# Performance work log

Hardware: AMD Instinct MI355X
Metric: run time of the kernel (lower is better)

## Reference

```python
import jax, jax.numpy as jnp
import numpy as np

N_HEADS = 8
HEAD_C = 48
NC = N_HEADS * HEAD_C  # 384
N_GROUPS = 4
GC = NC // N_GROUPS  # 96
STRIDE = 2
EPS = 1e-5


def conv1x1(x, w, b):
    # x: (B,C,H,W), w: (O,C), b: (O,)
    return jnp.einsum('bchw,oc->bohw', x, w) + b[None, :, None, None]


def ref_points(Hk, Wk, dtype):
    ry = jnp.linspace(0.5, Hk - 0.5, Hk, dtype=dtype) / (Hk - 1.0) * 2.0 - 1.0
    rx = jnp.linspace(0.5, Wk - 0.5, Wk, dtype=dtype) / (Wk - 1.0) * 2.0 - 1.0
    return jnp.stack(jnp.meshgrid(ry, rx, indexing='ij'), axis=-1)  # (Hk,Wk,2) in (y,x)


def grid_sample_bilinear(img, grid):
    # img: (N,C,H,W); grid: (N,Hg,Wg,2) xy in [-1,1]; align_corners=True, zeros padding
    N, C, H, W = img.shape
    gx = (grid[..., 0] + 1.0) * 0.5 * (W - 1)
    gy = (grid[..., 1] + 1.0) * 0.5 * (H - 1)
    x0 = jnp.floor(gx); y0 = jnp.floor(gy)
    x1 = x0 + 1.0;      y1 = y0 + 1.0
    wx1 = gx - x0; wx0 = 1.0 - wx1
    wy1 = gy - y0; wy0 = 1.0 - wy1

    def gather(ix, iy):
        valid = (ix >= 0) & (ix <= W - 1) & (iy >= 0) & (iy <= H - 1)
        ixc = jnp.clip(ix, 0, W - 1).astype(jnp.int32)
        iyc = jnp.clip(iy, 0, H - 1).astype(jnp.int32)
        vals = jax.vmap(lambda im, yy, xx: im[:, yy, xx])(img, iyc, ixc)  # (N,C,Hg,Wg)
        return vals * valid[:, None].astype(img.dtype)

    v00 = gather(x0, y0); v01 = gather(x1, y0)
    v10 = gather(x0, y1); v11 = gather(x1, y1)
    return (v00 * (wx0 * wy0)[:, None] + v01 * (wx1 * wy0)[:, None]
            + v10 * (wx0 * wy1)[:, None] + v11 * (wx1 * wy1)[:, None])


def _forward(x, Wq, bq, Wk, bk, Wv, bv, Wo, bo,
             off_dw_w, off_dw_b, ln_g, ln_b, off_pw_w):
    B, C, H, W = x.shape
    q = conv1x1(x, Wq, bq)                               # (B,C,H,W)
    q_off = q.reshape(B * N_GROUPS, GC, H, W)
    # offset net: depthwise 3x3 stride-2 conv -> channel LN -> GELU -> 1x1 to 2 ch
    h = jax.lax.conv_general_dilated(
        q_off, off_dw_w, (STRIDE, STRIDE), ((1, 1), (1, 1)),
        dimension_numbers=('NCHW', 'OIHW', 'NCHW'), feature_group_count=GC)
    h = h + off_dw_b[None, :, None, None]
    mu = h.mean(axis=1, keepdims=True)
    var = ((h - mu) ** 2).mean(axis=1, keepdims=True)
    h = (h - mu) / jnp.sqrt(var + EPS) * ln_g[None, :, None, None] + ln_b[None, :, None, None]
    h = jax.nn.gelu(h, approximate=False)
    offset = jnp.einsum('bchw,oc->bohw', h, off_pw_w)    # (B*g, 2, Hk, Wk), ch0=y, ch1=x
    Hk, Wk_ = offset.shape[2], offset.shape[3]
    rng = jnp.array([1.0 / (Hk - 1.0), 1.0 / (Wk_ - 1.0)], x.dtype).reshape(1, 2, 1, 1)
    offset = jnp.tanh(offset) * rng                      # offset_range_factor = 1
    offset = offset.transpose(0, 2, 3, 1)                # (B*g, Hk, Wk, 2) yx
    ref = ref_points(Hk, Wk_, x.dtype)                   # (Hk, Wk, 2) yx
    pos = offset + ref[None]
    xs = grid_sample_bilinear(x.reshape(B * N_GROUPS, GC, H, W), pos[..., ::-1])
    n = Hk * Wk_
    xs = xs.reshape(B, C, 1, n)
    k = conv1x1(xs, Wk, bk).reshape(B * N_HEADS, HEAD_C, n)
    v = conv1x1(xs, Wv, bv).reshape(B * N_HEADS, HEAD_C, n)
    qh = q.reshape(B * N_HEADS, HEAD_C, H * W)
    attn = jnp.einsum('bcm,bcn->bmn', qh, k) * (HEAD_C ** -0.5)
    attn = jax.nn.softmax(attn, axis=2)
    out = jnp.einsum('bmn,bcn->bcm', attn, v).reshape(B, C, H, W)
    y = conv1x1(out, Wo, bo)
    ref_b = jnp.broadcast_to(ref[None, None], (B, N_GROUPS, Hk, Wk_, 2))
    return y, pos.reshape(B, N_GROUPS, Hk, Wk_, 2), ref_b


def setup_inputs() -> dict:
    key = jax.random.key(0)
    ks = jax.random.split(key, 12)
    s = 0.02
    return {
        'x': jax.random.normal(ks[0], (8, NC, 56, 56), jnp.float32),
        'Wq': jax.random.normal(ks[1], (NC, NC), jnp.float32) * s,
        'bq': jnp.zeros((NC,), jnp.float32),
        'Wk': jax.random.normal(ks[2], (NC, NC), jnp.float32) * s,
        'bk': jnp.zeros((NC,), jnp.float32),
        'Wv': jax.random.normal(ks[3], (NC, NC), jnp.float32) * s,
        'bv': jnp.zeros((NC,), jnp.float32),
        'Wo': jax.random.normal(ks[4], (NC, NC), jnp.float32) * s,
        'bo': jnp.zeros((NC,), jnp.float32),
        'off_dw_w': jax.random.normal(ks[5], (GC, 1, 3, 3), jnp.float32) * 0.1,
        'off_dw_b': jnp.zeros((GC,), jnp.float32),
        'ln_g': jnp.ones((GC,), jnp.float32),
        'ln_b': jnp.zeros((GC,), jnp.float32),
        'off_pw_w': jax.random.normal(ks[6], (2, GC), jnp.float32) * 0.1,
    }


def reference(x, Wq, bq, Wk, bk, Wv, bv, Wo, bo,
              off_dw_w, off_dw_b, ln_g, ln_b, off_pw_w):
    return _forward(x, Wq, bq, Wk, bk, Wv, bv, Wo, bo,
                    off_dw_w, off_dw_b, ln_g, ln_b, off_pw_w)
```

## Files before the change

### kernel.cpp

```cpp
#include <hip/hip_runtime.h>
#include <math.h>

constexpr int BATCH = 8;
constexpr int NC    = 384;
constexpr int H     = 56, W = 56, HW = 3136;
constexpr int NPTS  = 784;
constexpr int NG    = 4, GC = 96;
constexpr int NH    = 8, HC = 48;

typedef __attribute__((ext_vector_type(8))) short short8;
typedef __attribute__((ext_vector_type(4))) float f32x4;
typedef __attribute__((ext_vector_type(4))) unsigned short us4;

__device__ inline unsigned short f2bf(float f) {
    union { float f; unsigned u; } v; v.f = f;
    unsigned r = v.u + 0x7FFF + ((v.u >> 16) & 1);
    return (unsigned short)(r >> 16);
}
__device__ inline unsigned short f2bf_t(float f) {
    union { float f; unsigned u; } v; v.f = f;
    return (unsigned short)(v.u >> 16);
}
__device__ inline float bf2f(unsigned short u) {
    union { unsigned u; float f; } v; v.u = (unsigned)u << 16;
    return v.f;
}
__device__ inline float wred_sum(float v) {
    #pragma unroll
    for (int off = 32; off > 0; off >>= 1) v += __shfl_xor(v, off);
    return v;
}

__global__ __launch_bounds__(256) void transpose_cvt(
    const float* __restrict__ x, unsigned short* __restrict__ xT)
{
    __shared__ unsigned short Ls[64 * 68];
    int b = blockIdx.z, c0 = blockIdx.y * 64, hw0 = blockIdx.x * 64;
    const float* xb = x + ((size_t)b * NC + c0) * HW + hw0;
    int t = threadIdx.x;
    #pragma unroll
    for (int i = 0; i < 4; i++) {
        int u = t + i * 256;
        int cc = u >> 4, f4 = (u & 15) * 4;
        float4 v = *(const float4*)&xb[(size_t)cc * HW + f4];
        us4 p; p[0] = f2bf(v.x); p[1] = f2bf(v.y); p[2] = f2bf(v.z); p[3] = f2bf(v.w);
        *(us4*)&Ls[cc * 68 + f4] = p;
    }
    __syncthreads();
    unsigned short* xTb = xT + ((size_t)b * HW + hw0) * NC + c0;
    #pragma unroll
    for (int i = 0; i < 4; i++) {
        int u = t + i * 256;
        int hw = u >> 4, cg = (u & 15) * 4;
        us4 p;
        p[0] = Ls[(cg + 0) * 68 + hw];
        p[1] = Ls[(cg + 1) * 68 + hw];
        p[2] = Ls[(cg + 2) * 68 + hw];
        p[3] = Ls[(cg + 3) * 68 + hw];
        *(us4*)&xTb[(size_t)hw * NC + cg] = p;
    }
}

__global__ __launch_bounds__(256) void wcvt(
    const float* __restrict__ w0, const float* __restrict__ w1,
    const float* __restrict__ w2, const float* __restrict__ w3,
    unsigned short* __restrict__ o0, unsigned short* __restrict__ okv,
    unsigned short* __restrict__ o3)
{
    const float* src; unsigned short* dst;
    switch (blockIdx.y) {
        case 0: src = w0; dst = o0; break;
        case 1: src = w1; dst = okv; break;
        case 2: src = w2; dst = okv + NC * NC; break;
        default: src = w3; dst = o3; break;
    }
    int idx = (blockIdx.x * 256 + threadIdx.x) * 4;
    float4 v = *(const float4*)&src[idx];
    us4 p; p[0] = f2bf(v.x); p[1] = f2bf(v.y); p[2] = f2bf(v.z); p[3] = f2bf(v.w);
    *(us4*)&dst[idx] = p;
}

template<int MODE>
__global__ __launch_bounds__(256) void gemm_bf16(
    const unsigned short* __restrict__ A, const float* __restrict__ bias,
    const float* __restrict__ bias2, const unsigned short* __restrict__ BT,
    float* __restrict__ Cf, unsigned short* __restrict__ Cb,
    unsigned short* __restrict__ Cb2, int N)
{
    int b  = blockIdx.z;
    int n0 = blockIdx.x * 128;
    int m0 = blockIdx.y * 128;
    const unsigned short* BTb = BT + (size_t)b * N * NC;

    __shared__ unsigned short As[128 * 40];
    __shared__ unsigned short Bs[128 * 40];

    int t = threadIdx.x;
    int wave = t >> 6, lane = t & 63;
    int quad = lane >> 4, col = lane & 15;
    int wm = (wave >> 1) * 64, wn = (wave & 1) * 64;

    const short8 z8 = {0,0,0,0,0,0,0,0};
    f32x4 acc[4][4];
    #pragma unroll
    for (int i = 0; i < 4; i++)
        #pragma unroll
        for (int j = 0; j < 4; j++) acc[i][j] = (f32x4){0.f, 0.f, 0.f, 0.f};

    for (int k0 = 0; k0 < NC; k0 += 32) {
        #pragma unroll
        for (int i = 0; i < 2; i++) {
            int u = t + i * 256;
            int mm = u >> 2, kc = (u & 3) * 8;
            *(short8*)&As[mm * 40 + kc] =
                *(const short8*)&A[(size_t)(m0 + mm) * NC + k0 + kc];
        }
        #pragma unroll
        for (int i = 0; i < 2; i++) {
            int u = t + i * 256;
            int nn = u >> 2, kc = (u & 3) * 8;
            short8 val = z8;
            if (n0 + nn < N)
                val = *(const short8*)&BTb[(size_t)(n0 + nn) * NC + k0 + kc];
            *(short8*)&Bs[nn * 40 + kc] = val;
        }
        __syncthreads();

        short8 af[4], bf[4];
        #pragma unroll
        for (int mt = 0; mt < 4; mt++)
            af[mt] = *(const short8*)&As[(wm + mt * 16 + col) * 40 + quad * 8];
        #pragma unroll
        for (int nt = 0; nt < 4; nt++)
            bf[nt] = *(const short8*)&Bs[(wn + nt * 16 + col) * 40 + quad * 8];
        #pragma unroll
        for (int mt = 0; mt < 4; mt++)
            #pragma unroll
            for (int nt = 0; nt < 4; nt++)
                acc[mt][nt] = __builtin_amdgcn_mfma_f32_16x16x32_bf16(
                    af[mt], bf[nt], acc[mt][nt], 0, 0, 0);
        __syncthreads();
    }

    if constexpr (MODE == 0) {
        float* Cfb = Cf + (size_t)b * NC * N;
        #pragma unroll
        for (int mt = 0; mt < 4; mt++) {
            #pragma unroll
            for (int r = 0; r < 4; r++) {
                int m = m0 + wm + mt * 16 + quad * 4 + r;
                float bv = bias[m];
                #pragma unroll
                for (int nt = 0; nt < 4; nt++) {
                    int n = n0 + wn + nt * 16 + col;
                    if (n < N) Cfb[(size_t)m * N + n] = acc[mt][nt][r] + bv;
                }
            }
        }
    } else if constexpr (MODE == 2) {
        unsigned short* Kb = Cb + (size_t)b * N * NC;
        #pragma unroll
        for (int mt = 0; mt < 4; mt++) {
            int mb = m0 + wm + mt * 16 + quad * 4;
            float bv[4];
            #pragma unroll
            for (int r = 0; r < 4; r++) bv[r] = bias[mb + r];
            #pragma unroll
            for (int nt = 0; nt < 4; nt++) {
                int n = n0 + wn + nt * 16 + col;
                if (n < N) {
                    us4 p;
                    #pragma unroll
                    for (int r = 0; r < 4; r++) p[r] = f2bf(acc[mt][nt][r] + bv[r]);
                    *(us4*)&Kb[(size_t)n * NC + mb] = p;
                }
            }
        }
    } else {
        if (m0 < NC) {
            unsigned short* Kb = Cb + (size_t)b * N * NC;
            #pragma unroll
            for (int mt = 0; mt < 4; mt++) {
                int mb = m0 + wm + mt * 16 + quad * 4;
                float bv[4];
                #pragma unroll
                for (int r = 0; r < 4; r++) bv[r] = bias[mb + r];
                #pragma unroll
                for (int nt = 0; nt < 4; nt++) {
                    int n = n0 + wn + nt * 16 + col;
                    if (n < N) {
                        us4 p;
                        #pragma unroll
                        for (int r = 0; r < 4; r++) p[r] = f2bf(acc[mt][nt][r] + bv[r]);
                        *(us4*)&Kb[(size_t)n * NC + mb] = p;
                    }
                }
            }
        } else {
            unsigned short* Vb = Cb2 + (size_t)b * NC * N;
            #pragma unroll
            for (int mt = 0; mt < 4; mt++) {
                #pragma unroll
                for (int r = 0; r < 4; r++) {
                    int m = m0 - NC + wm + mt * 16 + quad * 4 + r;
                    float bv = bias2[m];
                    #pragma unroll
                    for (int nt = 0; nt < 4; nt++) {
                        int n = n0 + wn + nt * 16 + col;
                        if (n < N) Vb[(size_t)m * N + n] = f2bf(acc[mt][nt][r] + bv);
                    }
                }
            }
        }
    }
}

__global__ __launch_bounds__(256) void offset_kernel(
    const unsigned short* __restrict__ qT, const float* __restrict__ dww,
    const float* __restrict__ dwb, const float* __restrict__ lng,
    const float* __restrict__ lnb, const float* __restrict__ pww,
    float* __restrict__ pos_out,   float* __restrict__ ref_out)
{
    int wave = threadIdx.x >> 6, l = threadIdx.x & 63;
    int bg = blockIdx.y, b = bg >> 2, g = bg & 3;
    int s  = blockIdx.x * 4 + wave;
    int py = s / 28, px = s - py * 28;
    bool has2 = l < 32;
    int c0 = l, c1 = 64 + l;

    const unsigned short* qb = qT + (size_t)b * HW * NC + g * GC;

    float h0 = 0.f, h1 = 0.f;
    #pragma unroll
    for (int ky = 0; ky < 3; ky++) {
        int yy = py * 2 - 1 + ky;
        if (yy < 0 || yy >= H) continue;
        #pragma unroll
        for (int kx = 0; kx < 3; kx++) {
            int xx = px * 2 - 1 + kx;
            if (xx < 0 || xx >= W) continue;
            const unsigned short* row = qb + (size_t)(yy * W + xx) * NC;
            float w0 = dww[c0 * 9 + ky * 3 + kx];
            h0 = fmaf(bf2f(row[c0]), w0, h0);
            if (has2) {
                float w1 = dww[c1 * 9 + ky * 3 + kx];
                h1 = fmaf(bf2f(row[c1]), w1, h1);
            }
        }
    }
    h0 += dwb[c0];
    if (has2) h1 += dwb[c1];

    float mu = wred_sum(h0 + (has2 ? h1 : 0.f)) * (1.f / GC);
    float d0 = h0 - mu, d1 = h1 - mu;
    float var = wred_sum(d0 * d0 + (has2 ? d1 * d1 : 0.f)) * (1.f / GC);
    float rstd = rsqrtf(var + 1e-5f);

    float hn0 = d0 * rstd * lng[c0] + lnb[c0];
    float ge0 = 0.5f * hn0 * (1.f + erff(hn0 * 0.70710678118654752f));
    float ge1 = 0.f;
    if (has2) {
        float hn1 = d1 * rstd * lng[c1] + lnb[c1];
        ge1 = 0.5f * hn1 * (1.f + erff(hn1 * 0.70710678118654752f));
    }

    float offy = wred_sum(ge0 * pww[c0] + (has2 ? ge1 * pww[c1] : 0.f));
    float offx = wred_sum(ge0 * pww[GC + c0] + (has2 ? ge1 * pww[GC + c1] : 0.f));

    if (l == 0) {
        float ry = (2.f * py + 1.f) / 27.f - 1.f;
        float rx = (2.f * px + 1.f) / 27.f - 1.f;
        size_t idx = ((size_t)bg * NPTS + s) * 2;
        pos_out[idx]     = tanhf(offy) * (1.f / 27.f) + ry;
        pos_out[idx + 1] = tanhf(offx) * (1.f / 27.f) + rx;
        ref_out[idx]     = ry;
        ref_out[idx + 1] = rx;
    }
}

__global__ __launch_bounds__(256) void sample_kernel(
    const unsigned short* __restrict__ xT, const float* __restrict__ pos,
    unsigned short* __restrict__ xsT)
{
    int bg = blockIdx.y;
    int b  = bg >> 2, g = bg & 3;
    int s  = blockIdx.x * 8 + (threadIdx.x >> 5);
    int l  = threadIdx.x & 31;

    const float* pg = pos + ((size_t)bg * NPTS + s) * 2;
    float py = pg[0], px = pg[1];
    float gx = (px + 1.f) * 27.5f;
    float gy = (py + 1.f) * 27.5f;
    float x0f = floorf(gx), y0f = floorf(gy);
    int ix0 = (int)x0f, iy0 = (int)y0f;
    int ix1 = ix0 + 1,  iy1 = iy0 + 1;
    float wx1 = gx - x0f, wx0 = 1.f - wx1;
    float wy1 = gy - y0f, wy0 = 1.f - wy1;
    bool vx0 = (ix0 >= 0) && (ix0 < W);
    bool vx1 = (ix1 >= 0) && (ix1 < W);
    bool vy0 = (iy0 >= 0) && (iy0 < H);
    bool vy1 = (iy1 >= 0) && (iy1 < H);
    int cx0 = vx0 ? ix0 : 0, cx1 = vx1 ? ix1 : 0;
    int cy0 = vy0 ? iy0 : 0, cy1 = vy1 ? iy1 : 0;
    float w00 = (vx0 && vy0) ? wx0 * wy0 : 0.f;
    float w01 = (vx1 && vy0) ? wx1 * wy0 : 0.f;
    float w10 = (vx0 && vy1) ? wx0 * wy1 : 0.f;
    float w11 = (vx1 && vy1) ? wx1 * wy1 : 0.f;

    const unsigned short* xb = xT + (size_t)b * HW * NC + g * GC;
    const unsigned short* r00 = xb + (size_t)(cy0 * W + cx0) * NC;
    const unsigned short* r01 = xb + (size_t)(cy0 * W + cx1) * NC;
    const unsigned short* r10 = xb + (size_t)(cy1 * W + cx0) * NC;
    const unsigned short* r11 = xb + (size_t)(cy1 * W + cx1) * NC;
    unsigned short* orow = xsT + ((size_t)b * NPTS + s) * NC + g * GC;
    #pragma unroll
    for (int ci = 0; ci < 3; ci++) {
        int c = l + ci * 32;
        float val = bf2f(r00[c]) * w00 + bf2f(r01[c]) * w01
                  + bf2f(r10[c]) * w10 + bf2f(r11[c]) * w11;
        orow[c] = f2bf(val);
    }
}

#define KS_STRIDE 56
#define VS_STRIDE 136
#define PS_STRIDE 40

__device__ inline short8 scale8(short8 v, float s) {
    short8 r;
    #pragma unroll
    for (int j = 0; j < 8; j++)
        r[j] = (short)f2bf(bf2f((unsigned short)v[j]) * s);
    return r;
}

__global__ __launch_bounds__(256) void attn_mfma(
    const unsigned short* __restrict__ qT, const unsigned short* __restrict__ kt,
    const unsigned short* __restrict__ vt, unsigned short* __restrict__ aoT)
{
    __shared__ __align__(16) unsigned short smem[23936];
    unsigned short* Ks = smem;
    unsigned short* Vs = Ks + 128 * KS_STRIDE;
    unsigned short* Ps = Vs + 48 * VS_STRIDE;

    int t    = threadIdx.x;
    int wave = t >> 6, lane = t & 63;
    int quad = lane >> 4, col = lane & 15;

    int bh = blockIdx.y;
    int b  = bh >> 3, h = bh & 7;
    int m0 = blockIdx.x * 256;
    const unsigned short* KT = kt + (size_t)b * NPTS * NC + h * HC;
    const unsigned short* VT = vt + ((size_t)b * NC + h * HC) * NPTS;

    const float scale = 0.14433756729740643f;
    const short8 z8 = {0,0,0,0,0,0,0,0};

    int gmq[4];
    short8 qb0[4], qb1[4];
    #pragma unroll
    for (int set = 0; set < 4; set++) {
        int gm = m0 + wave * 64 + set * 16 + col;
        gmq[set] = gm;
        int cg = gm < HW ? gm : HW - 1;
        const unsigned short* r0 = qT + ((size_t)b * HW + cg) * NC + h * HC;
        qb0[set] = scale8(*(const short8*)&r0[quad * 8], scale);
        qb1[set] = (quad < 2) ? scale8(*(const short8*)&r0[32 + quad * 8], scale) : z8;
    }

    unsigned short* paneW = Ps + wave * 4 * 16 * PS_STRIDE;

    float l_acc[4] = {0.f, 0.f, 0.f, 0.f};
    f32x4 acc_o[4][3];
    #pragma unroll
    for (int set = 0; set < 4; set++)
        #pragma unroll
        for (int ct = 0; ct < 3; ct++) acc_o[set][ct] = (f32x4){0.f, 0.f, 0.f, 0.f};

    int skey  = t >> 1;
    int spart = (t & 1) * 3;
    short8 kreg[3], vreg[3];

    {
        bool kv = skey < NPTS;
        const unsigned short* krow = KT + (size_t)skey * NC + spart * 8;
        #pragma unroll
        for (int i = 0; i < 3; i++) kreg[i] = kv ? *(const short8*)(krow + i * 8) : z8;
        #pragma unroll
        for (int i = 0; i < 3; i++) {
            int li = t + i * 256;
            int chan = li >> 4, part = li & 15;
            vreg[i] = *(const short8*)&VT[(size_t)chan * NPTS + part * 8];
        }
    }

    for (int ci = 0; ci < 7; ci++) {
        int k0 = ci * 128;

        #pragma unroll
        for (int i = 0; i < 3; i++)
            *(short8*)&Ks[skey * KS_STRIDE + (spart + i) * 8] = kreg[i];
        #pragma unroll
        for (int i = 0; i < 3; i++) {
            int li = t + i * 256;
            int chan = li >> 4, part = li & 15;
            *(short8*)&Vs[chan * VS_STRIDE + part * 8] = vreg[i];
        }
        __syncthreads();

        if (ci < 6) {
            int nk0 = k0 + 128;
            bool kv = nk0 + skey < NPTS;
            const unsigned short* krow = KT + (size_t)(nk0 + skey) * NC + spart * 8;
            #pragma unroll
            for (int i = 0; i < 3; i++) kreg[i] = kv ? *(const short8*)(krow + i * 8) : z8;
            #pragma unroll
            for (int i = 0; i < 3; i++) {
                int li = t + i * 256;
                int chan = li >> 4, part = li & 15;
                vreg[i] = (nk0 + part * 8 < NPTS)
                    ? *(const short8*)&VT[(size_t)chan * NPTS + nk0 + part * 8] : z8;
            }
        }

        #pragma unroll
        for (int s2 = 0; s2 < 4; s2++) {
            #pragma unroll
            for (int jth = 0; jth < 2; jth++) {
                int jt = s2 * 2 + jth;
                int keyl = jt * 16 + col;
                short8 kb0 = *(const short8*)&Ks[keyl * KS_STRIDE + quad * 8];
                short8 kb1 = (quad < 2)
                    ? *(const short8*)&Ks[keyl * KS_STRIDE + 32 + quad * 8] : z8;
                bool valid = (k0 + jt * 16) < NPTS;
                #pragma unroll
                for (int set = 0; set < 4; set++) {
                    f32x4 sa = {0.f, 0.f, 0.f, 0.f};
                    sa = __builtin_amdgcn_mfma_f32_16x16x32_bf16(kb0, qb0[set], sa, 0, 0, 0);
                    sa = __builtin_amdgcn_mfma_f32_16x16x32_bf16(kb1, qb1[set], sa, 0, 0, 0);
                    us4 p = {0, 0, 0, 0};
                    if (valid) {
                        #pragma unroll
                        for (int r = 0; r < 4; r++) {
                            float pv = __expf(sa[r]);
                            l_acc[set] += pv;
                            p[r] = f2bf_t(pv);
                        }
                    }
                    *(us4*)&paneW[set * 16 * PS_STRIDE + col * PS_STRIDE + jth * 16 + quad * 4] = p;
                }
            }
            short8 pb[4];
            #pragma unroll
            for (int set = 0; set < 4; set++)
                pb[set] = *(const short8*)&paneW[set * 16 * PS_STRIDE + col * PS_STRIDE + quad * 8];
            #pragma unroll
            for (int ct = 0; ct < 3; ct++) {
                short8 va = *(const short8*)&Vs[(ct * 16 + col) * VS_STRIDE + s2 * 32 + quad * 8];
                #pragma unroll
                for (int set = 0; set < 4; set++)
                    acc_o[set][ct] = __builtin_amdgcn_mfma_f32_16x16x32_bf16(
                        va, pb[set], acc_o[set][ct], 0, 0, 0);
            }
        }
        __syncthreads();
    }

    #pragma unroll
    for (int set = 0; set < 4; set++) {
        float l = l_acc[set];
        l += __shfl_xor(l, 16);
        l += __shfl_xor(l, 32);
        float inv = 1.f / l;
        int gm = gmq[set];
        if (gm < HW) {
            unsigned short* orow = aoT + ((size_t)b * HW + gm) * NC + h * HC;
            #pragma unroll
            for (int ct = 0; ct < 3; ct++) {
                us4 p;
                #pragma unroll
                for (int r = 0; r < 4; r++) p[r] = f2bf(acc_o[set][ct][r] * inv);
                *(us4*)&orow[ct * 16 + quad * 4] = p;
            }
        }
    }
}

extern "C" void kernel_launch(void* const* d_in, const int* in_sizes, int n_in,
                              void* d_out, int out_size, void* d_ws, size_t ws_size,
                              hipStream_t stream)
{
    const float* x   = (const float*)d_in[0];
    const float* Wq  = (const float*)d_in[1];
    const float* bq  = (const float*)d_in[2];
    const float* Wk  = (const float*)d_in[3];
    const float* bk  = (const float*)d_in[4];
    const float* Wv  = (const float*)d_in[5];
    const float* bv  = (const float*)d_in[6];
    const float* Wo  = (const float*)d_in[7];
    const float* bo  = (const float*)d_in[8];
    const float* dww = (const float*)d_in[9];
    const float* dwb = (const float*)d_in[10];
    const float* lng = (const float*)d_in[11];
    const float* lnb = (const float*)d_in[12];
    const float* pww = (const float*)d_in[13];

    float* out     = (float*)d_out;
    float* y_out   = out;
    float* pos_out = out + (size_t)BATCH * NC * HW;
    float* ref_out = pos_out + (size_t)BATCH * NG * NPTS * 2;

    const size_t NBIG = (size_t)BATCH * NC * HW;
    const size_t NSML = (size_t)BATCH * NC * NPTS;

    unsigned short* xT   = (unsigned short*)d_ws;
    unsigned short* qT   = xT   + NBIG;
    unsigned short* xsT  = qT   + NBIG;
    unsigned short* kt_w = xsT  + NSML;
    unsigned short* vt_w = kt_w + NSML;
    unsigned short* aoT  = vt_w + NSML;
    unsigned short* wqb  = aoT  + NBIG;
    unsigned short* wob  = wqb + NC * NC;
    unsigned short* wkv  = wob + NC * NC;

    transpose_cvt<<<dim3(49, 6, BATCH), 256, 0, stream>>>(x, xT);
    wcvt<<<dim3(144, 4), 256, 0, stream>>>(Wq, Wk, Wv, Wo, wqb, wkv, wob);
    gemm_bf16<2><<<dim3(25, 3, BATCH), 256, 0, stream>>>(
        wqb, bq, nullptr, xT, nullptr, qT, nullptr, HW);
    offset_kernel<<<dim3(196, BATCH * NG), 256, 0, stream>>>(
        qT, dww, dwb, lng, lnb, pww, pos_out, ref_out);
    sample_kernel<<<dim3(98, BATCH * NG), 256, 0, stream>>>(xT, pos_out, xsT);
    gemm_bf16<4><<<dim3(7, 6, BATCH), 256, 0, stream>>>(
        wkv, bk, bv, xsT, nullptr, kt_w, vt_w, NPTS);
    attn_mfma<<<dim3((HW + 255) / 256, BATCH * NH), 256, 0, stream>>>(
        qT, kt_w, vt_w, aoT);
    gemm_bf16<0><<<dim3(25, 3, BATCH), 256, 0, stream>>>(
        wob, bo, nullptr, aoT, y_out, nullptr, nullptr, HW);
}
```

Baseline: 323.8 us.

## Keep softmax probabilities in registers by permuting the V operand k-order

Drops the per-wave shared-memory P staging pane. The exp'd scores are packed straight from the QK MFMA output registers into the B operand of the PV MFMA. To keep the reduction index consistent, V is read from LDS as two 4-element halves, offset by 16, that match the permuted key order. It also skips the whole 32-key slice when it lies past NPTS, and drops the bounds check on the first K load. This removes an LDS write/read round trip per slice and shrinks LDS use, which may help occupancy. In exchange, V reads become two narrower LDS loads.

Result: faster. 309.2 us (-4.5%).

```diff
diff --git a/kernel.cpp b/kernel.cpp
--- a/kernel.cpp
+++ b/kernel.cpp
@@ -324,7 +324,6 @@
 
 #define KS_STRIDE 56
 #define VS_STRIDE 136
-#define PS_STRIDE 40
 
 __device__ inline short8 scale8(short8 v, float s) {
     short8 r;
@@ -334,14 +333,15 @@
     return r;
 }
 
+union pun8 { short8 s8; us4 h[2]; };
+
 __global__ __launch_bounds__(256) void attn_mfma(
     const unsigned short* __restrict__ qT, const unsigned short* __restrict__ kt,
     const unsigned short* __restrict__ vt, unsigned short* __restrict__ aoT)
 {
-    __shared__ __align__(16) unsigned short smem[23936];
+    __shared__ __align__(16) unsigned short smem[128 * KS_STRIDE + 48 * VS_STRIDE];
     unsigned short* Ks = smem;
     unsigned short* Vs = Ks + 128 * KS_STRIDE;
-    unsigned short* Ps = Vs + 48 * VS_STRIDE;
 
     int t    = threadIdx.x;
     int wave = t >> 6, lane = t & 63;
@@ -368,8 +368,6 @@
         qb1[set] = (quad < 2) ? scale8(*(const short8*)&r0[32 + quad * 8], scale) : z8;
     }
 
-    unsigned short* paneW = Ps + wave * 4 * 16 * PS_STRIDE;
-
     float l_acc[4] = {0.f, 0.f, 0.f, 0.f};
     f32x4 acc_o[4][3];
     #pragma unroll
@@ -382,10 +380,9 @@
     short8 kreg[3], vreg[3];
 
     {
-        bool kv = skey < NPTS;
         const unsigned short* krow = KT + (size_t)skey * NC + spart * 8;
         #pragma unroll
-        for (int i = 0; i < 3; i++) kreg[i] = kv ? *(const short8*)(krow + i * 8) : z8;
+        for (int i = 0; i < 3; i++) kreg[i] = *(const short8*)(krow + i * 8);
         #pragma unroll
         for (int i = 0; i < 3; i++) {
             int li = t + i * 256;
@@ -425,42 +422,53 @@
 
         #pragma unroll
         for (int s2 = 0; s2 < 4; s2++) {
-            #pragma unroll
-            for (int jth = 0; jth < 2; jth++) {
-                int jt = s2 * 2 + jth;
-                int keyl = jt * 16 + col;
-                short8 kb0 = *(const short8*)&Ks[keyl * KS_STRIDE + quad * 8];
-                short8 kb1 = (quad < 2)
-                    ? *(const short8*)&Ks[keyl * KS_STRIDE + 32 + quad * 8] : z8;
-                bool valid = (k0 + jt * 16) < NPTS;
+            if (k0 + s2 * 32 < NPTS) {
+                us4 pk[4][2];
+                #pragma unroll
+                for (int jth = 0; jth < 2; jth++) {
+                    int jt = s2 * 2 + jth;
+                    int keyl = jt * 16 + col;
+                    short8 kb0 = *(const short8*)&Ks[keyl * KS_STRIDE + quad * 8];
+                    short8 kb1 = (quad < 2)
+                        ? *(const short8*)&Ks[keyl * KS_STRIDE + 32 + quad * 8] : z8;
+                    bool valid = (k0 + jt * 16) < NPTS;
+                    #pragma unroll
+                    for (int set = 0; set < 4; set++) {
+                        f32x4 sa = {0.f, 0.f, 0.f, 0.f};
+                        sa = __builtin_amdgcn_mfma_f32_16x16x32_bf16(kb0, qb0[set], sa, 0, 0, 0);
+                        sa = __builtin_amdgcn_mfma_f32_16x16x32_bf16(kb1, qb1[set], sa, 0, 0, 0);
+                        us4 p = {0, 0, 0, 0};
+                        if (valid) {
+                            float e0 = __expf(sa[0]);
+                            float e1 = __expf(sa[1]);
+                            float e2 = __expf(sa[2]);
+                            float e3 = __expf(sa[3]);
+                            l_acc[set] += (e0 + e1) + (e2 + e3);
+                            p[0] = f2bf_t(e0); p[1] = f2bf_t(e1);
+                            p[2] = f2bf_t(e2); p[3] = f2bf_t(e3);
+                        }
+                        pk[set][jth] = p;
+                    }
+                }
+                short8 pb[4];
                 #pragma unroll
                 for (int set = 0; set < 4; set++) {
-                    f32x4 sa = {0.f, 0.f, 0.f, 0.f};
-                    sa = __builtin_amdgcn_mfma_f32_16x16x32_bf16(kb0, qb0[set], sa, 0, 0, 0);
-                    sa = __builtin_amdgcn_mfma_f32_16x16x32_bf16(kb1, qb1[set], sa, 0, 0, 0);
-                    us4 p = {0, 0, 0, 0};
-                    if (valid) {
-                        #pragma unroll
-                        for (int r = 0; r < 4; r++) {
-                            float pv = __expf(sa[r]);
-                            l_acc[set] += pv;
-                            p[r] = f2bf_t(pv);
-                        }
-                    }
-                    *(us4*)&paneW[set * 16 * PS_STRIDE + col * PS_STRIDE + jth * 16 + quad * 4] = p;
-                }
-            }
-            short8 pb[4];
-            #pragma unroll
-            for (int set = 0; set < 4; set++)
-                pb[set] = *(const short8*)&paneW[set * 16 * PS_STRIDE + col * PS_STRIDE + quad * 8];
-            #pragma unroll
-            for (int ct = 0; ct < 3; ct++) {
-                short8 va = *(const short8*)&Vs[(ct * 16 + col) * VS_STRIDE + s2 * 32 + quad * 8];
-                #pragma unroll
-                for (int set = 0; set < 4; set++)
-                    acc_o[set][ct] = __builtin_amdgcn_mfma_f32_16x16x32_bf16(
-                        va, pb[set], acc_o[set][ct], 0, 0, 0);
+                    pun8 u; u.h[0] = pk[set][0]; u.h[1] = pk[set][1];
+                    pb[set] = u.s8;
+                }
+                #pragma unroll
+                for (int ct = 0; ct < 3; ct++) {
+                    const unsigned short* vrow =
+                        &Vs[(ct * 16 + col) * VS_STRIDE + s2 * 32 + quad * 4];
+                    pun8 uv;
+                    uv.h[0] = *(const us4*)vrow;
+                    uv.h[1] = *(const us4*)(vrow + 16);
+                    short8 va = uv.s8;
+                    #pragma unroll
+                    for (int set = 0; set < 4; set++)
+                        acc_o[set][ct] = __builtin_amdgcn_mfma_f32_16x16x32_bf16(
+                            va, pb[set], acc_o[set][ct], 0, 0, 0);
+                }
             }
         }
         __syncthreads();
```
